# Performance work log

Hardware: AMD Instinct MI355X
Metric: run time of the kernel (lower is better)

Reference implementation:

```python
import jax, jax.numpy as jnp
import numpy as np

N_DRUG = 20000
N_PROT = 30000
N = N_DRUG + N_PROT
F_DRUG = 128
F_PROT = 256
H = 64          # hidden_channels
OUT = 1         # out_channels
E = 1_600_000
L = 200_000
LAYERS = 3


def _lin_init(key, fan_in, fan_out):
    return jax.random.normal(key, (fan_in, fan_out), jnp.float32) / np.sqrt(fan_in)


def setup_inputs() -> dict:
    key = jax.random.key(0)
    ks = jax.random.split(key, 10)
    x_drug = jax.random.normal(ks[0], (N_DRUG, F_DRUG), jnp.float32)
    x_protein = jax.random.normal(ks[1], (N_PROT, F_PROT), jnp.float32)
    edge_index = jax.random.randint(ks[2], (2, E), 0, N, dtype=jnp.int64)
    edge_label_src = jax.random.randint(ks[3], (L,), 0, N_DRUG, dtype=jnp.int64)
    # protein label indices point into the concatenated [drug; protein] tensor
    edge_label_dst = jax.random.randint(ks[4], (L,), 0, N_PROT, dtype=jnp.int64) + N_DRUG
    W_drug = _lin_init(ks[5], F_DRUG, H)
    b_drug = jnp.zeros((H,), jnp.float32)
    W_prot = _lin_init(ks[6], F_PROT, H)
    b_prot = jnp.zeros((H,), jnp.float32)
    conv_W = jax.random.normal(ks[7], (LAYERS, H, H), jnp.float32) / np.sqrt(H)
    conv_b = jnp.zeros((LAYERS, H), jnp.float32)
    lin_W = _lin_init(ks[8], H, OUT)
    lin_b = jnp.zeros((OUT,), jnp.float32)
    return {
        "x_drug": x_drug, "x_protein": x_protein,
        "W_drug": W_drug, "b_drug": b_drug,
        "W_prot": W_prot, "b_prot": b_prot,
        "conv_W": conv_W, "conv_b": conv_b,
        "lin_W": lin_W, "lin_b": lin_b,
        "edge_index": edge_index,
        "edge_label_src": edge_label_src,
        "edge_label_dst": edge_label_dst,
    }


def reference(x_drug, x_protein, W_drug, b_drug, W_prot, b_prot,
              conv_W, conv_b, lin_W, lin_b,
              edge_index, edge_label_src, edge_label_dst):
    # type-specific input projections + relu
    hd = jax.nn.relu(x_drug @ W_drug + b_drug)
    hp = jax.nn.relu(x_protein @ W_prot + b_prot)
    x = jnp.concatenate([hd, hp], axis=0)  # [N, H]

    src, dst = edge_index[0], edge_index[1]
    # GCN normalization with self-loops: deg counts in-edges (by dst) + 1
    deg = jax.ops.segment_sum(jnp.ones_like(src, dtype=x.dtype), dst, num_segments=N) + 1.0
    dis = jax.lax.rsqrt(deg)               # deg >= 1 always
    edge_norm = (dis[src] * dis[dst])[:, None]   # [E, 1]
    self_norm = (dis * dis)[:, None]             # [N, 1]

    for l in range(LAYERS):
        xw = x @ conv_W[l]                                   # [N, H] dense GEMM
        agg = jax.ops.segment_sum(xw[src] * edge_norm, dst, num_segments=N)
        x = jax.nn.relu(agg + xw * self_norm + conv_b[l])

    # edge scoring head: gather endpoints, linear to 1, multiply, sigmoid
    sd = (x[edge_label_src] @ lin_W + lin_b)[:, 0]  # [L]
    sp = (x[edge_label_dst] @ lin_W + lin_b)[:, 0]  # [L]
    return jax.nn.sigmoid(sd * sp)
```

## Files before the change

kernel.cpp:

```cpp
#include <hip/hip_runtime.h>
#include <hip/hip_fp16.h>
#include <math.h>

#define N_DRUG 20000
#define N_PROT 30000
#define NN (N_DRUG + N_PROT)
#define F_DRUG 128
#define F_PROT 256
#define H 64
#define NE 1600000
#define NL 200000

#define NB_PROJD ((N_DRUG + 127) / 128)
#define NB_PROJP ((N_PROT + 127) / 128)
#define NB_CONV  ((NN + 255) / 256)
#define NBK1 256
#define CH   ((NE + NBK1 - 1) / NBK1)
#define NB_BKT ((NN + 255) / 256)

typedef _Float16 h8 __attribute__((ext_vector_type(8)));
typedef _Float16 h4 __attribute__((ext_vector_type(4)));
typedef float f32x4 __attribute__((ext_vector_type(4)));

#define MFMA16(a, b, c) __builtin_amdgcn_mfma_f32_16x16x32_f16((a), (b), (c), 0, 0, 0)

__global__ __launch_bounds__(256) void k_wprep(
    const float* __restrict__ Wd, const float* __restrict__ Wp,
    const float* __restrict__ cw,
    _Float16* __restrict__ wdt, _Float16* __restrict__ wpt,
    _Float16* __restrict__ cwt) {
    int i = blockIdx.x * 256 + threadIdx.x;
    if (i < 64 * F_DRUG) {
        int c = i / F_DRUG, k = i % F_DRUG;
        wdt[i] = (_Float16)Wd[k * H + c];
    }
    if (i < 64 * F_PROT) {
        int c = i / F_PROT, k = i % F_PROT;
        wpt[i] = (_Float16)Wp[k * H + c];
    }
    if (i < 3 * 64 * 64) {
        int l = i >> 12, r = i & 4095;
        int c = r >> 6, k = r & 63;
        cwt[i] = (_Float16)cw[(l << 12) + k * H + c];
    }
}

template <int F>
__device__ __forceinline__ void proj_direct(
    const float* __restrict__ X, const _Float16* __restrict__ Wt,
    const float* __restrict__ bias, __half* __restrict__ out,
    int rows, int row_off, int bid) {
    int l = threadIdx.x & 63, wvi = threadIdx.x >> 6;
    int lr = l & 15, lq = l >> 4;
    int r0 = bid * 128 + wvi * 32;
    f32x4 acc[2][4];
    #pragma unroll
    for (int rt = 0; rt < 2; ++rt)
        #pragma unroll
        for (int n = 0; n < 4; ++n) acc[rt][n] = (f32x4){0.f, 0.f, 0.f, 0.f};

    for (int k0 = 0; k0 < F; k0 += 64) {
        h8 af[4][2];
        #pragma unroll
        for (int n = 0; n < 4; ++n)
            #pragma unroll
            for (int kk = 0; kk < 2; ++kk)
                af[n][kk] = *(const h8*)&Wt[(size_t)(n * 16 + lr) * F + k0 + kk * 32 + lq * 8];
        #pragma unroll
        for (int rt = 0; rt < 2; ++rt) {
            int r = r0 + rt * 16 + lr;
            int rc = (r < rows) ? r : (rows - 1);
            h8 bf[2];
            #pragma unroll
            for (int kk = 0; kk < 2; ++kk) {
                const float* xp = X + (size_t)rc * F + k0 + kk * 32 + lq * 8;
                float4 a = *(const float4*)xp;
                float4 b = *(const float4*)(xp + 4);
                h8 t;
                t[0] = (_Float16)a.x; t[1] = (_Float16)a.y;
                t[2] = (_Float16)a.z; t[3] = (_Float16)a.w;
                t[4] = (_Float16)b.x; t[5] = (_Float16)b.y;
                t[6] = (_Float16)b.z; t[7] = (_Float16)b.w;
                bf[kk] = t;
            }
            #pragma unroll
            for (int n = 0; n < 4; ++n) {
                acc[rt][n] = MFMA16(af[n][0], bf[0], acc[rt][n]);
                acc[rt][n] = MFMA16(af[n][1], bf[1], acc[rt][n]);
            }
        }
    }
    #pragma unroll
    for (int rt = 0; rt < 2; ++rt) {
        int r = r0 + rt * 16 + lr;
        if (r < rows) {
            #pragma unroll
            for (int n = 0; n < 4; ++n) {
                int c = n * 16 + lq * 4;
                float4 bv = *(const float4*)&bias[c];
                h4 hv;
                hv[0] = (_Float16)fmaxf(acc[rt][n][0] + bv.x, 0.f);
                hv[1] = (_Float16)fmaxf(acc[rt][n][1] + bv.y, 0.f);
                hv[2] = (_Float16)fmaxf(acc[rt][n][2] + bv.z, 0.f);
                hv[3] = (_Float16)fmaxf(acc[rt][n][3] + bv.w, 0.f);
                *(h4*)((_Float16*)out + (size_t)(row_off + r) * H + c) = hv;
            }
        }
    }
}

__device__ __forceinline__ void conv_direct(
    const __half* __restrict__ xin, const _Float16* __restrict__ Wt,
    __half* __restrict__ xout, int bid) {
    int l = threadIdx.x & 63, wvi = threadIdx.x >> 6;
    int lr = l & 15, lq = l >> 4;
    const _Float16* xh = (const _Float16*)xin;
    h8 af[4][2];
    #pragma unroll
    for (int n = 0; n < 4; ++n)
        #pragma unroll
        for (int kk = 0; kk < 2; ++kk)
            af[n][kk] = *(const h8*)&Wt[(size_t)(n * 16 + lr) * 64 + kk * 32 + lq * 8];
    int r0 = bid * 256 + wvi * 64;
    #pragma unroll
    for (int rt = 0; rt < 4; ++rt) {
        int r = r0 + rt * 16 + lr;
        int rc = (r < NN) ? r : (NN - 1);
        h8 bf0 = *(const h8*)&xh[(size_t)rc * H + lq * 8];
        h8 bf1 = *(const h8*)&xh[(size_t)rc * H + 32 + lq * 8];
        f32x4 a[4];
        #pragma unroll
        for (int n = 0; n < 4; ++n) {
            a[n] = (f32x4){0.f, 0.f, 0.f, 0.f};
            a[n] = MFMA16(af[n][0], bf0, a[n]);
            a[n] = MFMA16(af[n][1], bf1, a[n]);
        }
        if (r < NN) {
            #pragma unroll
            for (int n = 0; n < 4; ++n) {
                int c = n * 16 + lq * 4;
                h4 hv;
                hv[0] = (_Float16)a[n][0]; hv[1] = (_Float16)a[n][1];
                hv[2] = (_Float16)a[n][2]; hv[3] = (_Float16)a[n][3];
                *(h4*)((_Float16*)xout + (size_t)r * H + c) = hv;
            }
        }
    }
}

__global__ __launch_bounds__(256) void k_front(
    const float* __restrict__ xd, const _Float16* __restrict__ wdt, const float* __restrict__ bd,
    const float* __restrict__ xp, const _Float16* __restrict__ wpt, const float* __restrict__ bp,
    const int* __restrict__ ei, unsigned* __restrict__ bhist, __half* __restrict__ xbuf) {
    __shared__ unsigned lh[256];
    int bid = blockIdx.x;
    if (bid < NB_PROJD) {
        proj_direct<F_DRUG>(xd, wdt, bd, xbuf, N_DRUG, 0, bid);
    } else if (bid < NB_PROJD + NB_PROJP) {
        proj_direct<F_PROT>(xp, wpt, bp, xbuf, N_PROT, N_DRUG, bid - NB_PROJD);
    } else {
        int blk = bid - NB_PROJD - NB_PROJP;
        int t = threadIdx.x;
        lh[t] = 0;
        __syncthreads();
        int eb = blk * CH, ee = min(NE, eb + CH);
        for (int e = eb + t; e < ee; e += 256)
            atomicAdd(&lh[((unsigned)ei[NE + e]) >> 8], 1u);
        __syncthreads();
        bhist[(size_t)t * NBK1 + blk] = lh[t];
    }
}

__global__ __launch_bounds__(256) void kA(const unsigned* __restrict__ bhist,
                                          unsigned* __restrict__ rsum) {
    __shared__ unsigned s[256];
    int j = blockIdx.x, t = threadIdx.x;
    s[t] = bhist[(size_t)j * NBK1 + t];
    __syncthreads();
    for (int off = 128; off; off >>= 1) {
        if (t < off) s[t] += s[t + off];
        __syncthreads();
    }
    if (t == 0) rsum[j] = s[0];
}

__global__ __launch_bounds__(256) void kB(const unsigned* __restrict__ rsum,
                                          unsigned* __restrict__ rbase) {
    __shared__ unsigned s[256];
    int t = threadIdx.x;
    unsigned c = rsum[t];
    s[t] = c;
    __syncthreads();
    for (int off = 1; off < 256; off <<= 1) {
        unsigned v = s[t]; unsigned u = (t >= off) ? s[t - off] : 0;
        __syncthreads(); s[t] = v + u; __syncthreads();
    }
    rbase[t] = s[t] - c;
    if (t == 255) rbase[256] = s[255];
}

__global__ __launch_bounds__(256) void kC(unsigned* __restrict__ bhist,
                                          const unsigned* __restrict__ rbase) {
    __shared__ unsigned s[256];
    int j = blockIdx.x, t = threadIdx.x;
    unsigned c = bhist[(size_t)j * NBK1 + t];
    s[t] = c;
    __syncthreads();
    for (int off = 1; off < 256; off <<= 1) {
        unsigned v = s[t]; unsigned u = (t >= off) ? s[t - off] : 0;
        __syncthreads(); s[t] = v + u; __syncthreads();
    }
    bhist[(size_t)j * NBK1 + t] = rbase[j] + s[t] - c;
}

__global__ __launch_bounds__(256) void k_part(
    const int* __restrict__ ei, const unsigned* __restrict__ base,
    unsigned* __restrict__ tmp,
    const __half* __restrict__ xbuf, const _Float16* __restrict__ cwt,
    __half* __restrict__ xwh) {
    __shared__ unsigned lcur[256];
    int bid = blockIdx.x;
    if (bid < NBK1) {
        int t = threadIdx.x;
        lcur[t] = base[(size_t)t * NBK1 + bid];
        __syncthreads();
        int eb = bid * CH, ee = min(NE, eb + CH);
        for (int e = eb + t; e < ee; e += 256) {
            unsigned s = (unsigned)ei[e];
            unsigned d = (unsigned)ei[NE + e];
            unsigned pos = atomicAdd(&lcur[d >> 8], 1u);
            tmp[pos] = ((d & 255u) << 16) | s;
        }
    } else {
        conv_direct(xbuf, cwt, xwh, bid - NBK1);
    }
}

__global__ __launch_bounds__(256) void k_csr(
    const unsigned* __restrict__ tmp, const unsigned* __restrict__ rbase,
    int* __restrict__ rp, float* __restrict__ dis,
    unsigned short* __restrict__ csr) {
    __shared__ unsigned lbin[256], lofs[256], lcur[256];
    int b = blockIdx.x, t = threadIdx.x;
    unsigned nb0 = rbase[b], nb1 = rbase[b + 1];
    lbin[t] = 0;
    __syncthreads();
    for (unsigned i = nb0 + t; i < nb1; i += 256)
        atomicAdd(&lbin[tmp[i] >> 16], 1u);
    __syncthreads();
    unsigned c = lbin[t];
    lofs[t] = c;
    __syncthreads();
    for (int off = 1; off < 256; off <<= 1) {
        unsigned v = lofs[t]; unsigned u = (t >= off) ? lofs[t - off] : 0;
        __syncthreads(); lofs[t] = v + u; __syncthreads();
    }
    unsigned r = nb0 + lofs[t] - c;
    int node = b * 256 + t;
    if (node < NN) {
        rp[node] = (int)r;
        dis[node] = rsqrtf((float)c + 1.0f);
    }
    lcur[t] = r;
    __syncthreads();
    for (unsigned i = nb0 + t; i < nb1; i += 256) {
        unsigned rec = tmp[i];
        unsigned pos = atomicAdd(&lcur[rec >> 16], 1u);
        csr[pos] = (unsigned short)(rec & 0xffffu);
    }
    if (b == 0 && t == 0) rp[NN] = NE;
}

__global__ __launch_bounds__(256) void k_conv(
    const __half* __restrict__ X, const _Float16* __restrict__ Wt, __half* __restrict__ out) {
    conv_direct(X, Wt, out, blockIdx.x);
}

template <bool LAST>
__global__ __launch_bounds__(256) void k_spmm(
    const int* __restrict__ rp, const unsigned short* __restrict__ csr,
    const float* __restrict__ dis, const __half* __restrict__ xw,
    const float* __restrict__ bias, __half* __restrict__ xout,
    const float* __restrict__ lw, const float* __restrict__ lb,
    float* __restrict__ y) {
    int lane = threadIdx.x & 63;
    int wrp = threadIdx.x >> 6;
    int d = blockIdx.x * 4 + wrp;
    if (d >= NN) return;
    int q = lane >> 4, g = lane & 15;
    int beg = rp[d], end = rp[d + 1];
    float dd = dis[d];
    const _Float16* xh = (const _Float16*)xw;
    float ax = 0.f, ay = 0.f, az = 0.f, aw = 0.f;

    int n = end - beg; if (n > 64) n = 64;
    int sv = 0; float wv = 0.f;
    if (lane < n) { sv = csr[beg + lane]; wv = dis[sv]; }
    for (int b0 = beg; b0 < end; ) {
        int nb = b0 + 64;
        int n2 = end - nb; if (n2 > 64) n2 = 64;
        int sv2 = 0; float wv2 = 0.f;
        if (n2 > 0 && lane < n2) { sv2 = csr[nb + lane]; wv2 = dis[sv2]; }
        int nsteps = (n + 3) >> 2;
        #pragma unroll 4
        for (int jj = 0; jj < nsteps; ++jj) {
            int idx = jj * 4 + q;
            int s = __shfl(sv, idx);
            float w = __shfl(wv, idx);
            h4 xv = *(const h4*)&xh[((unsigned)s << 6) + (g << 2)];
            ax += w * (float)xv[0];
            ay += w * (float)xv[1];
            az += w * (float)xv[2];
            aw += w * (float)xv[3];
        }
        b0 = nb; n = n2; sv = sv2; wv = wv2;
    }
    ax += __shfl_xor(ax, 16); ay += __shfl_xor(ay, 16);
    az += __shfl_xor(az, 16); aw += __shfl_xor(aw, 16);
    ax += __shfl_xor(ax, 32); ay += __shfl_xor(ay, 32);
    az += __shfl_xor(az, 32); aw += __shfl_xor(aw, 32);

    h4 xs = *(const h4*)&xh[((unsigned)d << 6) + (g << 2)];
    float4 bv = *(const float4*)&bias[g << 2];
    float sn = dd * dd;
    float vx = fmaxf(dd * ax + sn * (float)xs[0] + bv.x, 0.f);
    float vy = fmaxf(dd * ay + sn * (float)xs[1] + bv.y, 0.f);
    float vz = fmaxf(dd * az + sn * (float)xs[2] + bv.z, 0.f);
    float vw = fmaxf(dd * aw + sn * (float)xs[3] + bv.w, 0.f);
    if (LAST) {
        float4 lv = *(const float4*)&lw[g << 2];
        float t = vx * lv.x + vy * lv.y + vz * lv.z + vw * lv.w;
        #pragma unroll
        for (int off = 8; off; off >>= 1) t += __shfl_xor(t, off);
        if (lane == 0) y[d] = t + lb[0];
    } else if (q == 0) {
        h4 hv;
        hv[0] = (_Float16)vx; hv[1] = (_Float16)vy;
        hv[2] = (_Float16)vz; hv[3] = (_Float16)vw;
        *(h4*)((_Float16*)xout + ((size_t)d << 6) + (g << 2)) = hv;
    }
}

__global__ void k_out(const float* __restrict__ y, const int* __restrict__ ls,
                      const int* __restrict__ ld, float* __restrict__ out) {
    int e = blockIdx.x * blockDim.x + threadIdx.x;
    if (e < NL) {
        float z = y[ls[e]] * y[ld[e]];
        out[e] = 1.f / (1.f + __expf(-z));
    }
}

static inline size_t up256(size_t x) { return (x + 255) & ~(size_t)255; }

extern "C" void kernel_launch(void* const* d_in, const int* in_sizes, int n_in,
                              void* d_out, int out_size, void* d_ws, size_t ws_size,
                              hipStream_t stream) {
    const float* x_drug = (const float*)d_in[0];
    const float* x_prot = (const float*)d_in[1];
    const float* W_drug = (const float*)d_in[2];
    const float* b_drug = (const float*)d_in[3];
    const float* W_prot = (const float*)d_in[4];
    const float* b_prot = (const float*)d_in[5];
    const float* conv_W = (const float*)d_in[6];
    const float* conv_b = (const float*)d_in[7];
    const float* lin_W  = (const float*)d_in[8];
    const float* lin_b  = (const float*)d_in[9];
    const int*   ei     = (const int*)d_in[10];
    const int*   lsrc   = (const int*)d_in[11];
    const int*   ldst   = (const int*)d_in[12];
    float* out = (float*)d_out;

    char* w = (char*)d_ws;
    size_t off = 0;
    unsigned* bhist = (unsigned*)(w + off); off = up256(off + (size_t)256 * NBK1 * 4);
    unsigned* rsum  = (unsigned*)(w + off); off = up256(off + 256 * 4);
    unsigned* rbase = (unsigned*)(w + off); off = up256(off + 257 * 4);
    unsigned* tmp   = (unsigned*)(w + off); off = up256(off + (size_t)NE * 4);
    unsigned short* csr = (unsigned short*)(w + off); off = up256(off + (size_t)NE * 2);
    int*    rp   = (int*)(w + off);    off = up256(off + (size_t)(NN + 1) * 4);
    float*  dis  = (float*)(w + off);  off = up256(off + (size_t)NN * 4);
    __half* xbuf = (__half*)(w + off); off = up256(off + (size_t)NN * H * 2);
    __half* xwh  = (__half*)(w + off); off = up256(off + (size_t)NN * H * 2);
    float*  y    = (float*)(w + off);  off = up256(off + (size_t)NN * 4);
    _Float16* wdt = (_Float16*)(w + off); off = up256(off + (size_t)64 * F_DRUG * 2);
    _Float16* wpt = (_Float16*)(w + off); off = up256(off + (size_t)64 * F_PROT * 2);
    _Float16* cwt = (_Float16*)(w + off); off = up256(off + (size_t)3 * 64 * 64 * 2);

    k_wprep<<<64, 256, 0, stream>>>(W_drug, W_prot, conv_W, wdt, wpt, cwt);

    k_front<<<NB_PROJD + NB_PROJP + NBK1, 256, 0, stream>>>(
        x_drug, wdt, b_drug, x_prot, wpt, b_prot, ei, bhist, xbuf);

    kA<<<256, 256, 0, stream>>>(bhist, rsum);
    kB<<<1, 256, 0, stream>>>(rsum, rbase);
    kC<<<256, 256, 0, stream>>>(bhist, rbase);

    k_part<<<NBK1 + NB_CONV, 256, 0, stream>>>(ei, bhist, tmp, xbuf, cwt, xwh);

    k_csr<<<NB_BKT, 256, 0, stream>>>(tmp, rbase, rp, dis, csr);

    k_spmm<false><<<(NN + 3) / 4, 256, 0, stream>>>(
        rp, csr, dis, xwh, conv_b, xbuf, nullptr, nullptr, nullptr);
    k_conv<<<NB_CONV, 256, 0, stream>>>(xbuf, cwt + 4096, xwh);
    k_spmm<false><<<(NN + 3) / 4, 256, 0, stream>>>(
        rp, csr, dis, xwh, conv_b + H, xbuf, nullptr, nullptr, nullptr);
    k_conv<<<NB_CONV, 256, 0, stream>>>(xbuf, cwt + 8192, xwh);
    k_spmm<true><<<(NN + 3) / 4, 256, 0, stream>>>(
        rp, csr, dis, xwh, conv_b + 2 * H, nullptr, lin_W, lin_b, y);

    k_out<<<(NL + 255) / 256, 256, 0, stream>>>(y, lsrc, ldst, out);
}
```

Before: 208.1 us.

## Precompute packed per-edge source index and fp16 edge weight for SpMM

```diff
diff --git a/kernel.cpp b/kernel.cpp
--- a/kernel.cpp
+++ b/kernel.cpp
@@ -14,6 +14,7 @@
 #define NB_PROJD ((N_DRUG + 127) / 128)
 #define NB_PROJP ((N_PROT + 127) / 128)
 #define NB_CONV  ((NN + 255) / 256)
+#define NB_ROW4  ((NN + 3) / 4)
 #define NBK1 256
 #define CH   ((NE + NBK1 - 1) / NBK1)
 #define NB_BKT ((NN + 255) / 256)
@@ -215,24 +216,18 @@
 
 __global__ __launch_bounds__(256) void k_part(
     const int* __restrict__ ei, const unsigned* __restrict__ base,
-    unsigned* __restrict__ tmp,
-    const __half* __restrict__ xbuf, const _Float16* __restrict__ cwt,
-    __half* __restrict__ xwh) {
+    unsigned* __restrict__ tmp) {
     __shared__ unsigned lcur[256];
     int bid = blockIdx.x;
-    if (bid < NBK1) {
-        int t = threadIdx.x;
-        lcur[t] = base[(size_t)t * NBK1 + bid];
-        __syncthreads();
-        int eb = bid * CH, ee = min(NE, eb + CH);
-        for (int e = eb + t; e < ee; e += 256) {
-            unsigned s = (unsigned)ei[e];
-            unsigned d = (unsigned)ei[NE + e];
-            unsigned pos = atomicAdd(&lcur[d >> 8], 1u);
-            tmp[pos] = ((d & 255u) << 16) | s;
-        }
-    } else {
-        conv_direct(xbuf, cwt, xwh, bid - NBK1);
+    int t = threadIdx.x;
+    lcur[t] = base[(size_t)t * NBK1 + bid];
+    __syncthreads();
+    int eb = bid * CH, ee = min(NE, eb + CH);
+    for (int e = eb + t; e < ee; e += 256) {
+        unsigned s = (unsigned)ei[e];
+        unsigned d = (unsigned)ei[NE + e];
+        unsigned pos = atomicAdd(&lcur[d >> 8], 1u);
+        tmp[pos] = ((d & 255u) << 16) | s;
     }
 }
 
@@ -271,6 +266,29 @@
     if (b == 0 && t == 0) rp[NN] = NE;
 }
 
+__global__ __launch_bounds__(256) void k_pc(
+    const int* __restrict__ rp, const unsigned short* __restrict__ csr,
+    const float* __restrict__ dis, unsigned* __restrict__ pack,
+    const __half* __restrict__ xbuf, const _Float16* __restrict__ cwt,
+    __half* __restrict__ xwh) {
+    int bid = blockIdx.x;
+    if (bid < NB_CONV) {
+        conv_direct(xbuf, cwt, xwh, bid);
+    } else {
+        int d = (bid - NB_CONV) * 4 + (threadIdx.x >> 6);
+        if (d >= NN) return;
+        int lane = threadIdx.x & 63;
+        int beg = rp[d], end = rp[d + 1];
+        float dd = dis[d];
+        for (int i = beg + lane; i < end; i += 64) {
+            int s = csr[i];
+            float w = dis[s] * dd;
+            pack[i] = (unsigned)s |
+                      ((unsigned)__half_as_ushort(__float2half(w)) << 16);
+        }
+    }
+}
+
 __global__ __launch_bounds__(256) void k_conv(
     const __half* __restrict__ X, const _Float16* __restrict__ Wt, __half* __restrict__ out) {
     conv_direct(X, Wt, out, blockIdx.x);
@@ -278,55 +296,54 @@
 
 template <bool LAST>
 __global__ __launch_bounds__(256) void k_spmm(
-    const int* __restrict__ rp, const unsigned short* __restrict__ csr,
+    const int* __restrict__ rp, const unsigned* __restrict__ pack,
     const float* __restrict__ dis, const __half* __restrict__ xw,
     const float* __restrict__ bias, __half* __restrict__ xout,
     const float* __restrict__ lw, const float* __restrict__ lb,
     float* __restrict__ y) {
     int lane = threadIdx.x & 63;
-    int wrp = threadIdx.x >> 6;
-    int d = blockIdx.x * 4 + wrp;
+    int d = blockIdx.x * 4 + (threadIdx.x >> 6);
     if (d >= NN) return;
     int q = lane >> 4, g = lane & 15;
     int beg = rp[d], end = rp[d + 1];
-    float dd = dis[d];
     const _Float16* xh = (const _Float16*)xw;
     float ax = 0.f, ay = 0.f, az = 0.f, aw = 0.f;
 
     int n = end - beg; if (n > 64) n = 64;
-    int sv = 0; float wv = 0.f;
-    if (lane < n) { sv = csr[beg + lane]; wv = dis[sv]; }
+    unsigned rv = 0;
+    if (lane < n) rv = pack[beg + lane];
     for (int b0 = beg; b0 < end; ) {
         int nb = b0 + 64;
         int n2 = end - nb; if (n2 > 64) n2 = 64;
-        int sv2 = 0; float wv2 = 0.f;
-        if (n2 > 0 && lane < n2) { sv2 = csr[nb + lane]; wv2 = dis[sv2]; }
+        unsigned rv2 = 0;
+        if (n2 > 0 && lane < n2) rv2 = pack[nb + lane];
         int nsteps = (n + 3) >> 2;
         #pragma unroll 4
         for (int jj = 0; jj < nsteps; ++jj) {
-            int idx = jj * 4 + q;
-            int s = __shfl(sv, idx);
-            float w = __shfl(wv, idx);
+            unsigned r = __shfl(rv, jj * 4 + q);
+            int s = (int)(r & 0xffffu);
+            float w = __half2float(__ushort_as_half((unsigned short)(r >> 16)));
             h4 xv = *(const h4*)&xh[((unsigned)s << 6) + (g << 2)];
             ax += w * (float)xv[0];
             ay += w * (float)xv[1];
             az += w * (float)xv[2];
             aw += w * (float)xv[3];
         }
-        b0 = nb; n = n2; sv = sv2; wv = wv2;
+        b0 = nb; n = n2; rv = rv2;
     }
     ax += __shfl_xor(ax, 16); ay += __shfl_xor(ay, 16);
     az += __shfl_xor(az, 16); aw += __shfl_xor(aw, 16);
     ax += __shfl_xor(ax, 32); ay += __shfl_xor(ay, 32);
     az += __shfl_xor(az, 32); aw += __shfl_xor(aw, 32);
 
+    float dd = dis[d];
+    float sn = dd * dd;
     h4 xs = *(const h4*)&xh[((unsigned)d << 6) + (g << 2)];
     float4 bv = *(const float4*)&bias[g << 2];
-    float sn = dd * dd;
-    float vx = fmaxf(dd * ax + sn * (float)xs[0] + bv.x, 0.f);
-    float vy = fmaxf(dd * ay + sn * (float)xs[1] + bv.y, 0.f);
-    float vz = fmaxf(dd * az + sn * (float)xs[2] + bv.z, 0.f);
-    float vw = fmaxf(dd * aw + sn * (float)xs[3] + bv.w, 0.f);
+    float vx = fmaxf(ax + sn * (float)xs[0] + bv.x, 0.f);
+    float vy = fmaxf(ay + sn * (float)xs[1] + bv.y, 0.f);
+    float vz = fmaxf(az + sn * (float)xs[2] + bv.z, 0.f);
+    float vw = fmaxf(aw + sn * (float)xs[3] + bv.w, 0.f);
     if (LAST) {
         float4 lv = *(const float4*)&lw[g << 2];
         float t = vx * lv.x + vy * lv.y + vz * lv.z + vw * lv.w;
@@ -377,6 +394,7 @@
     unsigned* rbase = (unsigned*)(w + off); off = up256(off + 257 * 4);
     unsigned* tmp   = (unsigned*)(w + off); off = up256(off + (size_t)NE * 4);
     unsigned short* csr = (unsigned short*)(w + off); off = up256(off + (size_t)NE * 2);
+    unsigned* pack  = (unsigned*)(w + off); off = up256(off + (size_t)NE * 4);
     int*    rp   = (int*)(w + off);    off = up256(off + (size_t)(NN + 1) * 4);
     float*  dis  = (float*)(w + off);  off = up256(off + (size_t)NN * 4);
     __half* xbuf = (__half*)(w + off); off = up256(off + (size_t)NN * H * 2);
@@ -395,18 +413,20 @@
     kB<<<1, 256, 0, stream>>>(rsum, rbase);
     kC<<<256, 256, 0, stream>>>(bhist, rbase);
 
-    k_part<<<NBK1 + NB_CONV, 256, 0, stream>>>(ei, bhist, tmp, xbuf, cwt, xwh);
+    k_part<<<NBK1, 256, 0, stream>>>(ei, bhist, tmp);
 
     k_csr<<<NB_BKT, 256, 0, stream>>>(tmp, rbase, rp, dis, csr);
 
-    k_spmm<false><<<(NN + 3) / 4, 256, 0, stream>>>(
-        rp, csr, dis, xwh, conv_b, xbuf, nullptr, nullptr, nullptr);
+    k_pc<<<NB_CONV + NB_ROW4, 256, 0, stream>>>(rp, csr, dis, pack, xbuf, cwt, xwh);
+
+    k_spmm<false><<<NB_ROW4, 256, 0, stream>>>(
+        rp, pack, dis, xwh, conv_b, xbuf, nullptr, nullptr, nullptr);
     k_conv<<<NB_CONV, 256, 0, stream>>>(xbuf, cwt + 4096, xwh);
-    k_spmm<false><<<(NN + 3) / 4, 256, 0, stream>>>(
-        rp, csr, dis, xwh, conv_b + H, xbuf, nullptr, nullptr, nullptr);
+    k_spmm<false><<<NB_ROW4, 256, 0, stream>>>(
+        rp, pack, dis, xwh, conv_b + H, xbuf, nullptr, nullptr, nullptr);
     k_conv<<<NB_CONV, 256, 0, stream>>>(xbuf, cwt + 8192, xwh);
-    k_spmm<true><<<(NN + 3) / 4, 256, 0, stream>>>(
-        rp, csr, dis, xwh, conv_b + 2 * H, nullptr, lin_W, lin_b, y);
+    k_spmm<true><<<NB_ROW4, 256, 0, stream>>>(
+        rp, pack, dis, xwh, conv_b + 2 * H, nullptr, lin_W, lin_b, y);
 
     k_out<<<(NL + 255) / 256, 256, 0, stream>>>(y, lsrc, ldst, out);
 }
```

After: 214.0 us. 2.8% more time.

## Aggregate before transform: fuse conv GEMM into SpMM, pack edge weights, merge scans

Applied to the files above, without the earlier changes.

```diff
diff --git a/kernel.cpp b/kernel.cpp
--- a/kernel.cpp
+++ b/kernel.cpp
@@ -13,7 +13,7 @@
 
 #define NB_PROJD ((N_DRUG + 127) / 128)
 #define NB_PROJP ((N_PROT + 127) / 128)
-#define NB_CONV  ((NN + 255) / 256)
+#define NB_ROW4  (NN / 4)
 #define NBK1 256
 #define CH   ((NE + NBK1 - 1) / NBK1)
 #define NB_BKT ((NN + 255) / 256)
@@ -39,16 +39,14 @@
         wpt[i] = (_Float16)Wp[k * H + c];
     }
     if (i < 3 * 64 * 64) {
-        int l = i >> 12, r = i & 4095;
-        int c = r >> 6, k = r & 63;
-        cwt[i] = (_Float16)cw[(l << 12) + k * H + c];
+        cwt[i] = (_Float16)cw[i];
     }
 }
 
 template <int F>
 __device__ __forceinline__ void proj_direct(
     const float* __restrict__ X, const _Float16* __restrict__ Wt,
-    const float* __restrict__ bias, __half* __restrict__ out,
+    const float* __restrict__ bias, _Float16* __restrict__ out,
     int rows, int row_off, int bid) {
     int l = threadIdx.x & 63, wvi = threadIdx.x >> 6;
     int lr = l & 15, lq = l >> 4;
@@ -103,46 +101,7 @@
                 hv[1] = (_Float16)fmaxf(acc[rt][n][1] + bv.y, 0.f);
                 hv[2] = (_Float16)fmaxf(acc[rt][n][2] + bv.z, 0.f);
                 hv[3] = (_Float16)fmaxf(acc[rt][n][3] + bv.w, 0.f);
-                *(h4*)((_Float16*)out + (size_t)(row_off + r) * H + c) = hv;
-            }
-        }
-    }
-}
-
-__device__ __forceinline__ void conv_direct(
-    const __half* __restrict__ xin, const _Float16* __restrict__ Wt,
-    __half* __restrict__ xout, int bid) {
-    int l = threadIdx.x & 63, wvi = threadIdx.x >> 6;
-    int lr = l & 15, lq = l >> 4;
-    const _Float16* xh = (const _Float16*)xin;
-    h8 af[4][2];
-    #pragma unroll
-    for (int n = 0; n < 4; ++n)
-        #pragma unroll
-        for (int kk = 0; kk < 2; ++kk)
-            af[n][kk] = *(const h8*)&Wt[(size_t)(n * 16 + lr) * 64 + kk * 32 + lq * 8];
-    int r0 = bid * 256 + wvi * 64;
-    #pragma unroll
-    for (int rt = 0; rt < 4; ++rt) {
-        int r = r0 + rt * 16 + lr;
-        int rc = (r < NN) ? r : (NN - 1);
-        h8 bf0 = *(const h8*)&xh[(size_t)rc * H + lq * 8];
-        h8 bf1 = *(const h8*)&xh[(size_t)rc * H + 32 + lq * 8];
-        f32x4 a[4];
-        #pragma unroll
-        for (int n = 0; n < 4; ++n) {
-            a[n] = (f32x4){0.f, 0.f, 0.f, 0.f};
-            a[n] = MFMA16(af[n][0], bf0, a[n]);
-            a[n] = MFMA16(af[n][1], bf1, a[n]);
-        }
-        if (r < NN) {
-            #pragma unroll
-            for (int n = 0; n < 4; ++n) {
-                int c = n * 16 + lq * 4;
-                h4 hv;
-                hv[0] = (_Float16)a[n][0]; hv[1] = (_Float16)a[n][1];
-                hv[2] = (_Float16)a[n][2]; hv[3] = (_Float16)a[n][3];
-                *(h4*)((_Float16*)xout + (size_t)r * H + c) = hv;
+                *(h4*)(out + (size_t)(row_off + r) * H + c) = hv;
             }
         }
     }
@@ -151,13 +110,13 @@
 __global__ __launch_bounds__(256) void k_front(
     const float* __restrict__ xd, const _Float16* __restrict__ wdt, const float* __restrict__ bd,
     const float* __restrict__ xp, const _Float16* __restrict__ wpt, const float* __restrict__ bp,
-    const int* __restrict__ ei, unsigned* __restrict__ bhist, __half* __restrict__ xbuf) {
+    const int* __restrict__ ei, unsigned* __restrict__ bhist, _Float16* __restrict__ xa) {
     __shared__ unsigned lh[256];
     int bid = blockIdx.x;
     if (bid < NB_PROJD) {
-        proj_direct<F_DRUG>(xd, wdt, bd, xbuf, N_DRUG, 0, bid);
+        proj_direct<F_DRUG>(xd, wdt, bd, xa, N_DRUG, 0, bid);
     } else if (bid < NB_PROJD + NB_PROJP) {
-        proj_direct<F_PROT>(xp, wpt, bp, xbuf, N_PROT, N_DRUG, bid - NB_PROJD);
+        proj_direct<F_PROT>(xp, wpt, bp, xa, N_PROT, N_DRUG, bid - NB_PROJD);
     } else {
         int blk = bid - NB_PROJD - NB_PROJP;
         int t = threadIdx.x;
@@ -184,55 +143,48 @@
     if (t == 0) rsum[j] = s[0];
 }
 
-__global__ __launch_bounds__(256) void kB(const unsigned* __restrict__ rsum,
-                                          unsigned* __restrict__ rbase) {
-    __shared__ unsigned s[256];
-    int t = threadIdx.x;
-    unsigned c = rsum[t];
+__global__ __launch_bounds__(256) void kC2(unsigned* __restrict__ bhist,
+                                           const unsigned* __restrict__ rsum,
+                                           unsigned* __restrict__ rbase) {
+    __shared__ unsigned sb[256], s[256];
+    int j = blockIdx.x, t = threadIdx.x;
+    unsigned rc = rsum[t];
+    sb[t] = rc;
+    __syncthreads();
+    for (int off = 1; off < 256; off <<= 1) {
+        unsigned v = sb[t]; unsigned u = (t >= off) ? sb[t - off] : 0;
+        __syncthreads(); sb[t] = v + u; __syncthreads();
+    }
+    if (j == 0) {
+        rbase[t] = sb[t] - rc;
+        if (t == 255) rbase[256] = sb[255];
+    }
+    unsigned rb = (j > 0) ? sb[j - 1] : 0;
+    unsigned c = bhist[(size_t)j * NBK1 + t];
     s[t] = c;
     __syncthreads();
     for (int off = 1; off < 256; off <<= 1) {
         unsigned v = s[t]; unsigned u = (t >= off) ? s[t - off] : 0;
         __syncthreads(); s[t] = v + u; __syncthreads();
     }
-    rbase[t] = s[t] - c;
-    if (t == 255) rbase[256] = s[255];
-}
-
-__global__ __launch_bounds__(256) void kC(unsigned* __restrict__ bhist,
-                                          const unsigned* __restrict__ rbase) {
-    __shared__ unsigned s[256];
-    int j = blockIdx.x, t = threadIdx.x;
-    unsigned c = bhist[(size_t)j * NBK1 + t];
-    s[t] = c;
-    __syncthreads();
-    for (int off = 1; off < 256; off <<= 1) {
-        unsigned v = s[t]; unsigned u = (t >= off) ? s[t - off] : 0;
-        __syncthreads(); s[t] = v + u; __syncthreads();
-    }
-    bhist[(size_t)j * NBK1 + t] = rbase[j] + s[t] - c;
+    bhist[(size_t)j * NBK1 + t] = rb + s[t] - c;
 }
 
 __global__ __launch_bounds__(256) void k_part(
     const int* __restrict__ ei, const unsigned* __restrict__ base,
-    unsigned* __restrict__ tmp,
-    const __half* __restrict__ xbuf, const _Float16* __restrict__ cwt,
-    __half* __restrict__ xwh) {
+    unsigned* __restrict__ tmp) {
     __shared__ unsigned lcur[256];
     int bid = blockIdx.x;
-    if (bid < NBK1) {
-        int t = threadIdx.x;
-        lcur[t] = base[(size_t)t * NBK1 + bid];
-        __syncthreads();
-        int eb = bid * CH, ee = min(NE, eb + CH);
-        for (int e = eb + t; e < ee; e += 256) {
-            unsigned s = (unsigned)ei[e];
-            unsigned d = (unsigned)ei[NE + e];
-            unsigned pos = atomicAdd(&lcur[d >> 8], 1u);
-            tmp[pos] = ((d & 255u) << 16) | s;
-        }
-    } else {
-        conv_direct(xbuf, cwt, xwh, bid - NBK1);
+    int c = ((bid & 7) << 5) | (bid >> 3);
+    int t = threadIdx.x;
+    lcur[t] = base[(size_t)t * NBK1 + c];
+    __syncthreads();
+    int eb = c * CH, ee = min(NE, eb + CH);
+    for (int e = eb + t; e < ee; e += 256) {
+        unsigned s = (unsigned)ei[e];
+        unsigned d = (unsigned)ei[NE + e];
+        unsigned pos = atomicAdd(&lcur[d >> 8], 1u);
+        tmp[pos] = ((d & 255u) << 16) | s;
     }
 }
 
@@ -271,73 +223,90 @@
     if (b == 0 && t == 0) rp[NN] = NE;
 }
 
-__global__ __launch_bounds__(256) void k_conv(
-    const __half* __restrict__ X, const _Float16* __restrict__ Wt, __half* __restrict__ out) {
-    conv_direct(X, Wt, out, blockIdx.x);
-}
-
-template <bool LAST>
-__global__ __launch_bounds__(256) void k_spmm(
+template <bool FIRST, bool LAST>
+__global__ __launch_bounds__(256) void k_spmm3(
     const int* __restrict__ rp, const unsigned short* __restrict__ csr,
-    const float* __restrict__ dis, const __half* __restrict__ xw,
-    const float* __restrict__ bias, __half* __restrict__ xout,
+    unsigned* __restrict__ pack, const float* __restrict__ dis,
+    const _Float16* __restrict__ xin, const _Float16* __restrict__ Wl,
+    const float* __restrict__ bias, _Float16* __restrict__ xout,
     const float* __restrict__ lw, const float* __restrict__ lb,
     float* __restrict__ y) {
-    int lane = threadIdx.x & 63;
-    int wrp = threadIdx.x >> 6;
+    __shared__ float rowbuf[4][64];
+    int lane = threadIdx.x & 63, wrp = threadIdx.x >> 6;
     int d = blockIdx.x * 4 + wrp;
-    if (d >= NN) return;
     int q = lane >> 4, g = lane & 15;
     int beg = rp[d], end = rp[d + 1];
     float dd = dis[d];
-    const _Float16* xh = (const _Float16*)xw;
     float ax = 0.f, ay = 0.f, az = 0.f, aw = 0.f;
 
-    int n = end - beg; if (n > 64) n = 64;
-    int sv = 0; float wv = 0.f;
-    if (lane < n) { sv = csr[beg + lane]; wv = dis[sv]; }
-    for (int b0 = beg; b0 < end; ) {
-        int nb = b0 + 64;
-        int n2 = end - nb; if (n2 > 64) n2 = 64;
-        int sv2 = 0; float wv2 = 0.f;
-        if (n2 > 0 && lane < n2) { sv2 = csr[nb + lane]; wv2 = dis[sv2]; }
-        int nsteps = (n + 3) >> 2;
-        #pragma unroll 4
-        for (int jj = 0; jj < nsteps; ++jj) {
-            int idx = jj * 4 + q;
-            int s = __shfl(sv, idx);
-            float w = __shfl(wv, idx);
-            h4 xv = *(const h4*)&xh[((unsigned)s << 6) + (g << 2)];
-            ax += w * (float)xv[0];
-            ay += w * (float)xv[1];
-            az += w * (float)xv[2];
-            aw += w * (float)xv[3];
+    #pragma unroll 4
+    for (int idx = beg + q; idx < end; idx += 4) {
+        int s; float w;
+        if (FIRST) {
+            s = csr[idx];
+            w = dis[s] * dd;
+            if (g == 0)
+                pack[idx] = (unsigned)s |
+                            ((unsigned)__half_as_ushort(__float2half(w)) << 16);
+        } else {
+            unsigned r = pack[idx];
+            s = (int)(r & 0xffffu);
+            w = __half2float(__ushort_as_half((unsigned short)(r >> 16)));
         }
-        b0 = nb; n = n2; sv = sv2; wv = wv2;
+        h4 xv = *(const h4*)&xin[((unsigned)s << 6) + (g << 2)];
+        ax += w * (float)xv[0];
+        ay += w * (float)xv[1];
+        az += w * (float)xv[2];
+        aw += w * (float)xv[3];
     }
     ax += __shfl_xor(ax, 16); ay += __shfl_xor(ay, 16);
     az += __shfl_xor(az, 16); aw += __shfl_xor(aw, 16);
     ax += __shfl_xor(ax, 32); ay += __shfl_xor(ay, 32);
     az += __shfl_xor(az, 32); aw += __shfl_xor(aw, 32);
-
-    h4 xs = *(const h4*)&xh[((unsigned)d << 6) + (g << 2)];
+    h4 xs = *(const h4*)&xin[((unsigned)d << 6) + (g << 2)];
+    float sn = dd * dd;
+    ax += sn * (float)xs[0]; ay += sn * (float)xs[1];
+    az += sn * (float)xs[2]; aw += sn * (float)xs[3];
+
+    if (q == 0) *(float4*)&rowbuf[wrp][g << 2] = make_float4(ax, ay, az, aw);
+    __syncthreads();
+    float o0 = 0.f, o1 = 0.f, o2 = 0.f, o3 = 0.f;
+    #pragma unroll
+    for (int t = 0; t < 4; ++t) {
+        int f0 = (q << 4) + (t << 2);
+        float4 rv = *(const float4*)&rowbuf[wrp][f0];
+        const float* rvp = (const float*)&rv;
+        #pragma unroll
+        for (int i = 0; i < 4; ++i) {
+            h4 wv = *(const h4*)&Wl[(size_t)(f0 + i) * 64 + (g << 2)];
+            float r = rvp[i];
+            o0 += r * (float)wv[0];
+            o1 += r * (float)wv[1];
+            o2 += r * (float)wv[2];
+            o3 += r * (float)wv[3];
+        }
+    }
+    o0 += __shfl_xor(o0, 16); o1 += __shfl_xor(o1, 16);
+    o2 += __shfl_xor(o2, 16); o3 += __shfl_xor(o3, 16);
+    o0 += __shfl_xor(o0, 32); o1 += __shfl_xor(o1, 32);
+    o2 += __shfl_xor(o2, 32); o3 += __shfl_xor(o3, 32);
+
     float4 bv = *(const float4*)&bias[g << 2];
-    float sn = dd * dd;
-    float vx = fmaxf(dd * ax + sn * (float)xs[0] + bv.x, 0.f);
-    float vy = fmaxf(dd * ay + sn * (float)xs[1] + bv.y, 0.f);
-    float vz = fmaxf(dd * az + sn * (float)xs[2] + bv.z, 0.f);
-    float vw = fmaxf(dd * aw + sn * (float)xs[3] + bv.w, 0.f);
+    float vx = fmaxf(o0 + bv.x, 0.f);
+    float vy = fmaxf(o1 + bv.y, 0.f);
+    float vz = fmaxf(o2 + bv.z, 0.f);
+    float vw = fmaxf(o3 + bv.w, 0.f);
     if (LAST) {
         float4 lv = *(const float4*)&lw[g << 2];
-        float t = vx * lv.x + vy * lv.y + vz * lv.z + vw * lv.w;
-        #pragma unroll
-        for (int off = 8; off; off >>= 1) t += __shfl_xor(t, off);
-        if (lane == 0) y[d] = t + lb[0];
+        float tt = vx * lv.x + vy * lv.y + vz * lv.z + vw * lv.w;
+        tt += __shfl_xor(tt, 1); tt += __shfl_xor(tt, 2);
+        tt += __shfl_xor(tt, 4); tt += __shfl_xor(tt, 8);
+        if (lane == 0) y[d] = tt + lb[0];
     } else if (q == 0) {
         h4 hv;
         hv[0] = (_Float16)vx; hv[1] = (_Float16)vy;
         hv[2] = (_Float16)vz; hv[3] = (_Float16)vw;
-        *(h4*)((_Float16*)xout + ((size_t)d << 6) + (g << 2)) = hv;
+        *(h4*)(xout + ((size_t)d << 6) + (g << 2)) = hv;
     }
 }
 
@@ -377,10 +346,11 @@
     unsigned* rbase = (unsigned*)(w + off); off = up256(off + 257 * 4);
     unsigned* tmp   = (unsigned*)(w + off); off = up256(off + (size_t)NE * 4);
     unsigned short* csr = (unsigned short*)(w + off); off = up256(off + (size_t)NE * 2);
+    unsigned* pack  = (unsigned*)(w + off); off = up256(off + (size_t)NE * 4);
     int*    rp   = (int*)(w + off);    off = up256(off + (size_t)(NN + 1) * 4);
     float*  dis  = (float*)(w + off);  off = up256(off + (size_t)NN * 4);
-    __half* xbuf = (__half*)(w + off); off = up256(off + (size_t)NN * H * 2);
-    __half* xwh  = (__half*)(w + off); off = up256(off + (size_t)NN * H * 2);
+    _Float16* xa = (_Float16*)(w + off); off = up256(off + (size_t)NN * H * 2);
+    _Float16* xb = (_Float16*)(w + off); off = up256(off + (size_t)NN * H * 2);
     float*  y    = (float*)(w + off);  off = up256(off + (size_t)NN * 4);
     _Float16* wdt = (_Float16*)(w + off); off = up256(off + (size_t)64 * F_DRUG * 2);
     _Float16* wpt = (_Float16*)(w + off); off = up256(off + (size_t)64 * F_PROT * 2);
@@ -389,24 +359,21 @@
     k_wprep<<<64, 256, 0, stream>>>(W_drug, W_prot, conv_W, wdt, wpt, cwt);
 
     k_front<<<NB_PROJD + NB_PROJP + NBK1, 256, 0, stream>>>(
-        x_drug, wdt, b_drug, x_prot, wpt, b_prot, ei, bhist, xbuf);
+        x_drug, wdt, b_drug, x_prot, wpt, b_prot, ei, bhist, xa);
 
     kA<<<256, 256, 0, stream>>>(bhist, rsum);
-    kB<<<1, 256, 0, stream>>>(rsum, rbase);
-    kC<<<256, 256, 0, stream>>>(bhist, rbase);
-
-    k_part<<<NBK1 + NB_CONV, 256, 0, stream>>>(ei, bhist, tmp, xbuf, cwt, xwh);
+    kC2<<<256, 256, 0, stream>>>(bhist, rsum, rbase);
+
+    k_part<<<NBK1, 256, 0, stream>>>(ei, bhist, tmp);
 
     k_csr<<<NB_BKT, 256, 0, stream>>>(tmp, rbase, rp, dis, csr);
 
-    k_spmm<false><<<(NN + 3) / 4, 256, 0, stream>>>(
-        rp, csr, dis, xwh, conv_b, xbuf, nullptr, nullptr, nullptr);
-    k_conv<<<NB_CONV, 256, 0, stream>>>(xbuf, cwt + 4096, xwh);
-    k_spmm<false><<<(NN + 3) / 4, 256, 0, stream>>>(
-        rp, csr, dis, xwh, conv_b + H, xbuf, nullptr, nullptr, nullptr);
-    k_conv<<<NB_CONV, 256, 0, stream>>>(xbuf, cwt + 8192, xwh);
-    k_spmm<true><<<(NN + 3) / 4, 256, 0, stream>>>(
-        rp, csr, dis, xwh, conv_b + 2 * H, nullptr, lin_W, lin_b, y);
+    k_spmm3<true, false><<<NB_ROW4, 256, 0, stream>>>(
+        rp, csr, pack, dis, xa, cwt, conv_b, xb, nullptr, nullptr, nullptr);
+    k_spmm3<false, false><<<NB_ROW4, 256, 0, stream>>>(
+        rp, csr, pack, dis, xb, cwt + 4096, conv_b + 64, xa, nullptr, nullptr, nullptr);
+    k_spmm3<false, true><<<NB_ROW4, 256, 0, stream>>>(
+        rp, csr, pack, dis, xa, cwt + 8192, conv_b + 128, nullptr, lin_W, lin_b, y);
 
     k_out<<<(NL + 255) / 256, 256, 0, stream>>>(y, lsrc, ldst, out);
 }
```

New measurement: 266.1 us. 27.9% more time.
